# Performance work log

Hardware: AMD Instinct MI355X
Metric: run time of the kernel (lower is better)

Reference implementation:

```python
import jax, jax.numpy as jnp
import numpy as np

THRESHOLD = 0.95


def setup_inputs() -> dict:
    key = jax.random.key(0)
    k1, k2 = jax.random.split(key, 2)
    B, T, D = 16, 2048, 1024
    hs = jax.random.normal(k1, (B, T, D), dtype=jnp.float32)
    hs_mask = jnp.ones((B, 1, T), dtype=jnp.float32)
    w = jax.random.normal(k2, (D,), dtype=jnp.float32) * 0.02  # project.weight [1,D] -> [D]
    b = jnp.zeros((), dtype=jnp.float32)                        # project.bias
    return {"hs": hs, "hs_mask": hs_mask, "w": w, "b": b}


def reference(hs, hs_mask, w, b):
    B, T, D = hs.shape
    # project + sigmoid + mask
    x = jnp.einsum("btd,d->bt", hs, w) + b            # [B,T]
    alphas_s = jax.nn.sigmoid(x)
    alphas = alphas_s * hs_mask[:, 0, :]              # [B,T]

    # ---- integrate-and-fire scan over time ----
    def step(carry, inp):
        integrate, frame = carry                      # [B], [B,D]
        alpha, h = inp                                # [B], [B,D]
        dist_completion = 1.0 - integrate
        integrate = integrate + alpha
        fire_val = integrate                          # recorded pre-reset value
        fireplace = integrate > THRESHOLD
        integrate = jnp.where(fireplace, integrate - 1.0, integrate)
        cur = jnp.where(fireplace, dist_completion, alpha)
        frame_out = frame + cur[:, None] * h          # recorded frame at t
        frame_next = jnp.where(fireplace[:, None], (alpha - cur)[:, None] * h, frame_out)
        return (integrate, frame_next), (fire_val, frame_out)

    init = (jnp.zeros((B,), hs.dtype), jnp.zeros((B, D), hs.dtype))
    _, (fires_t, frames_t) = jax.lax.scan(
        step, init, (jnp.swapaxes(alphas, 0, 1), jnp.swapaxes(hs, 0, 1)))
    fires = jnp.swapaxes(fires_t, 0, 1)               # [B,T]
    frames = jnp.swapaxes(frames_t, 0, 1)             # [B,T,D]

    # ---- gather fired frames, left-packed, padded to static L=T ----
    fired = fires > THRESHOLD                         # [B,T]
    pos = jnp.cumsum(fired.astype(jnp.int32), axis=1) - 1
    L = T                                             # static upper bound on label length
    pos = jnp.where(fired, pos, L)                    # out-of-range -> dropped
    bidx = jnp.broadcast_to(jnp.arange(B, dtype=jnp.int32)[:, None], (B, T))
    out = jnp.zeros((B, L, D), hs.dtype).at[bidx, pos].set(frames, mode="drop")

    len_labels = jnp.round(alphas.sum(-1)).astype(jnp.int32)          # [B]
    new_masks = (jnp.arange(L)[None, :] < len_labels[:, None])[:, None, :]  # [B,1,L] bool
    return out, new_masks
```

## Files before the change

### kernel.cpp

```cpp
#include <hip/hip_runtime.h>
#include <math.h>

#define BB 16
#define TT 2048
#define DD 1024
#define THRESH 0.95f

__global__ __launch_bounds__(256) void proj_kernel(
    const float* __restrict__ hs, const float* __restrict__ hs_mask,
    const float* __restrict__ w, const float* __restrict__ bias,
    float* __restrict__ alphas)
{
    int row  = blockIdx.x * 4 + (threadIdx.x >> 6);
    int lane = threadIdx.x & 63;
    const float4* hp = (const float4*)(hs + (size_t)row * DD);
    const float4* wp = (const float4*)w;
    float sum = 0.f;
#pragma unroll
    for (int j = 0; j < 4; ++j) {
        float4 h4 = hp[lane + 64 * j];
        float4 w4 = wp[lane + 64 * j];
        sum += h4.x * w4.x + h4.y * w4.y + h4.z * w4.z + h4.w * w4.w;
    }
#pragma unroll
    for (int off = 32; off; off >>= 1) sum += __shfl_down(sum, off, 64);
    if (lane == 0) {
        float x  = sum + bias[0];
        float al = 1.f / (1.f + expf(-x));
        alphas[row] = al * hs_mask[row];
    }
}


#define SCAN_GROUP(RREG, GIDX)                                                \
    {                                                                         \
        float cv = 0.f, pv = 0.f;                                             \
        _Pragma("unroll 16")                                                  \
        for (int j = 0; j < 64; ++j) {                                        \
            float a = __int_as_float(                                         \
                __builtin_amdgcn_readlane(__float_as_int(RREG), j));          \
            float pre  = integ + a;                         \
            bool  fire = pre > THRESH;                      \
            float c    = fire ? dist : a;                                     \
            integ      = fire ? pre - 1.f : pre;        \
            dist       = 1.f - integ;                                         \
            bool sel   = (lane == j);                                         \
            cv = sel ? c   : cv;                                              \
            pv = sel ? pre : pv;                                              \
        }                                                                     \
        cp[(GIDX) * 64 + lane] = cv;                                          \
        unsigned long long bm = __ballot(pv > THRESH);                        \
        gmask = (lane == (GIDX)) ? bm : gmask;                                \
    }

__global__ __launch_bounds__(64) void scan_kernel(
    const float* __restrict__ alphas, float* __restrict__ cur,
    int* __restrict__ fire_times, int* __restrict__ n_fires,
    int* __restrict__ len_labels)
{
    int b    = blockIdx.x;
    int lane = threadIdx.x;
    const float* ap = alphas + (size_t)b * TT;
    float*       cp = cur    + (size_t)b * TT;

    unsigned long long gmask = 0ull;
    float integ = 0.f, dist = 1.f;
    double dsum = 0.0;

    for (int outer = 0; outer < 4; ++outer) {
        int base = outer * 512 + lane;
        float r0 = ap[base +   0];
        float r1 = ap[base +  64];
        float r2 = ap[base + 128];
        float r3 = ap[base + 192];
        float r4 = ap[base + 256];
        float r5 = ap[base + 320];
        float r6 = ap[base + 384];
        float r7 = ap[base + 448];
        dsum += (double)r0 + (double)r1 + (double)r2 + (double)r3
              + (double)r4 + (double)r5 + (double)r6 + (double)r7;
        int gb = outer * 8;
        SCAN_GROUP(r0, gb + 0)
        SCAN_GROUP(r1, gb + 1)
        SCAN_GROUP(r2, gb + 2)
        SCAN_GROUP(r3, gb + 3)
        SCAN_GROUP(r4, gb + 4)
        SCAN_GROUP(r5, gb + 5)
        SCAN_GROUP(r6, gb + 6)
        SCAN_GROUP(r7, gb + 7)
    }

#pragma unroll
    for (int off = 32; off; off >>= 1) dsum += __shfl_down(dsum, off, 64);
    if (lane == 0) len_labels[b] = (int)__double2int_rn(dsum);

    int cnt  = __popcll(gmask);
    int pref = cnt;
#pragma unroll
    for (int off = 1; off < 64; off <<= 1) {
        int y = __shfl_up(pref, off, 64);
        if (lane >= off) pref += y;
    }
    int pos = pref - cnt;
    unsigned long long m = gmask;
    int baset = lane * 64;
    int* fp = fire_times + (size_t)b * TT;
    while (m) {
        int j = __ffsll(m) - 1;
        fp[pos++] = baset + j;
        m &= m - 1;
    }
    if (lane == 63) n_fires[b] = pref;
}

__global__ __launch_bounds__(256) void gather_kernel(
    const float* __restrict__ hs, const float* __restrict__ alphas,
    const float* __restrict__ cur, const int* __restrict__ fire_times,
    const int* __restrict__ n_fires, const int* __restrict__ len_labels,
    float* __restrict__ out, float* __restrict__ out_mask)
{
    int ro = blockIdx.x;
    int b  = ro >> 11;
    int r  = ro & (TT - 1);
    if (threadIdx.x == 0)
        out_mask[ro] = (r < len_labels[b]) ? 1.f : 0.f;

    float4* op = (float4*)(out + (size_t)ro * DD);
    int ti = threadIdx.x;
    if (r >= n_fires[b]) {
        float4 z = {0.f, 0.f, 0.f, 0.f};
        op[ti] = z;
        return;
    }
    int t_end  = fire_times[b * TT + r];
    int t_prev = r ? fire_times[b * TT + r - 1] : -1;

    const float4* hsb = (const float4*)(hs + (size_t)b * TT * DD);
    float4 acc = {0.f, 0.f, 0.f, 0.f};
    if (t_prev >= 0) {
        float c = alphas[b * TT + t_prev] - cur[b * TT + t_prev];
        float4 h = hsb[(size_t)t_prev * 256 + ti];
        acc.x += c * h.x; acc.y += c * h.y; acc.z += c * h.z; acc.w += c * h.w;
    }
    for (int t = t_prev + 1; t <= t_end; ++t) {
        float c = cur[b * TT + t];
        float4 h = hsb[(size_t)t * 256 + ti];
        acc.x += c * h.x; acc.y += c * h.y; acc.z += c * h.z; acc.w += c * h.w;
    }
    op[ti] = acc;
}

extern "C" void kernel_launch(void* const* d_in, const int* in_sizes, int n_in,
                              void* d_out, int out_size, void* d_ws, size_t ws_size,
                              hipStream_t stream) {
    const float* hs      = (const float*)d_in[0];
    const float* hs_mask = (const float*)d_in[1];
    const float* w       = (const float*)d_in[2];
    const float* bias    = (const float*)d_in[3];

    float* out      = (float*)d_out;
    float* out_mask = out + (size_t)BB * TT * DD;

    float* alphas     = (float*)d_ws;
    float* cur        = alphas + BB * TT;
    int*   fire_times = (int*)(cur + BB * TT);
    int*   n_fires    = fire_times + BB * TT;
    int*   len_labels = n_fires + BB;

    proj_kernel<<<BB * TT / 4, 256, 0, stream>>>(hs, hs_mask, w, bias, alphas);
    scan_kernel<<<BB, 64, 0, stream>>>(alphas, cur, fire_times, n_fires, len_labels);
    gather_kernel<<<BB * TT, 256, 0, stream>>>(hs, alphas, cur, fire_times,
                                               n_fires, len_labels, out, out_mask);
}
```

Measured before the change: 309.0 us.

## Process multiple output rows per gather block, reuse boundary frame, nontemporal stores

The gather kernel now handles 8 consecutive output rows per block. It walks the time range once and carries the boundary hidden row and its leftover weight from one fired frame to the next, so that row is not reloaded from memory. Output writes use nontemporal stores to avoid polluting the cache with the large output, and mask generation moves into the scan kernel. The trade-off is fewer, longer-running blocks with a serial dependency chain inside each block, which may cut parallelism and memory-level overlap.

```diff
diff --git a/kernel.cpp b/kernel.cpp
--- a/kernel.cpp
+++ b/kernel.cpp
@@ -5,6 +5,14 @@
 #define TT 2048
 #define DD 1024
 #define THRESH 0.95f
+#define RPB 8
+
+typedef float nt4 __attribute__((ext_vector_type(4)));
+
+__device__ __forceinline__ void nt_store4(const float4& v, float4* p) {
+    nt4 x = {v.x, v.y, v.z, v.w};
+    __builtin_nontemporal_store(x, (nt4*)p);
+}
 
 __global__ __launch_bounds__(256) void proj_kernel(
     const float* __restrict__ hs, const float* __restrict__ hs_mask,
@@ -56,7 +64,7 @@
 __global__ __launch_bounds__(64) void scan_kernel(
     const float* __restrict__ alphas, float* __restrict__ cur,
     int* __restrict__ fire_times, int* __restrict__ n_fires,
-    int* __restrict__ len_labels)
+    int* __restrict__ len_labels, float* __restrict__ out_mask)
 {
     int b    = blockIdx.x;
     int lane = threadIdx.x;
@@ -92,7 +100,14 @@
 
 #pragma unroll
     for (int off = 32; off; off >>= 1) dsum += __shfl_down(dsum, off, 64);
-    if (lane == 0) len_labels[b] = (int)__double2int_rn(dsum);
+    int len = __double2int_rn(dsum);
+    len = __shfl(len, 0, 64);
+    if (lane == 0) len_labels[b] = len;
+
+    float* mp = out_mask + (size_t)b * TT;
+#pragma unroll
+    for (int j = 0; j < TT / 64; ++j)
+        mp[j * 64 + lane] = ((j * 64 + lane) < len) ? 1.f : 0.f;
 
     int cnt  = __popcll(gmask);
     int pref = cnt;
@@ -116,38 +131,71 @@
 __global__ __launch_bounds__(256) void gather_kernel(
     const float* __restrict__ hs, const float* __restrict__ alphas,
     const float* __restrict__ cur, const int* __restrict__ fire_times,
-    const int* __restrict__ n_fires, const int* __restrict__ len_labels,
-    float* __restrict__ out, float* __restrict__ out_mask)
+    const int* __restrict__ n_fires, float* __restrict__ out)
 {
-    int ro = blockIdx.x;
-    int b  = ro >> 11;
-    int r  = ro & (TT - 1);
-    if (threadIdx.x == 0)
-        out_mask[ro] = (r < len_labels[b]) ? 1.f : 0.f;
-
-    float4* op = (float4*)(out + (size_t)ro * DD);
+    int chunk = blockIdx.x;
+    int b  = chunk >> 8;
+    int r0 = (chunk & 255) * RPB;
     int ti = threadIdx.x;
-    if (r >= n_fires[b]) {
+    int nf = n_fires[b];
+
+    float4* ob = (float4*)(out + ((size_t)b * TT + r0) * DD);
+
+    if (r0 >= nf) {
         float4 z = {0.f, 0.f, 0.f, 0.f};
-        op[ti] = z;
+#pragma unroll
+        for (int i = 0; i < RPB; ++i)
+            nt_store4(z, &ob[i * 256 + ti]);
         return;
     }
-    int t_end  = fire_times[b * TT + r];
-    int t_prev = r ? fire_times[b * TT + r - 1] : -1;
-
+
+    const int*    ft  = fire_times + (size_t)b * TT;
+    const float*  al  = alphas     + (size_t)b * TT;
+    const float*  cu  = cur        + (size_t)b * TT;
     const float4* hsb = (const float4*)(hs + (size_t)b * TT * DD);
-    float4 acc = {0.f, 0.f, 0.f, 0.f};
-    if (t_prev >= 0) {
-        float c = alphas[b * TT + t_prev] - cur[b * TT + t_prev];
-        float4 h = hsb[(size_t)t_prev * 256 + ti];
-        acc.x += c * h.x; acc.y += c * h.y; acc.z += c * h.z; acc.w += c * h.w;
-    }
-    for (int t = t_prev + 1; t <= t_end; ++t) {
-        float c = cur[b * TT + t];
-        float4 h = hsb[(size_t)t * 256 + ti];
-        acc.x += c * h.x; acc.y += c * h.y; acc.z += c * h.z; acc.w += c * h.w;
-    }
-    op[ti] = acc;
+
+    int    t;
+    float4 hprev = {0.f, 0.f, 0.f, 0.f};
+    float  wprev = 0.f;
+    bool   have_prev;
+    if (r0 == 0) {
+        t = 0;
+        have_prev = false;
+    } else {
+        int tp = ft[r0 - 1];
+        t = tp + 1;
+        hprev = hsb[(size_t)tp * 256 + ti];
+        wprev = al[tp] - cu[tp];
+        have_prev = true;
+    }
+
+#pragma unroll
+    for (int i = 0; i < RPB; ++i) {
+        int r = r0 + i;
+        float4 a = {0.f, 0.f, 0.f, 0.f};
+        if (r < nf) {
+            if (have_prev) {
+                a.x = wprev * hprev.x; a.y = wprev * hprev.y;
+                a.z = wprev * hprev.z; a.w = wprev * hprev.w;
+            }
+            int te = ft[r];
+            for (;;) {
+                float4 h  = hsb[(size_t)t * 256 + ti];
+                float  cw = cu[t];
+                a.x += cw * h.x; a.y += cw * h.y;
+                a.z += cw * h.z; a.w += cw * h.w;
+                if (t == te) {
+                    wprev = al[t] - cw;
+                    hprev = h;
+                    ++t;
+                    break;
+                }
+                ++t;
+            }
+            have_prev = true;
+        }
+        nt_store4(a, &ob[i * 256 + ti]);
+    }
 }
 
 extern "C" void kernel_launch(void* const* d_in, const int* in_sizes, int n_in,
@@ -168,7 +216,8 @@
     int*   len_labels = n_fires + BB;
 
     proj_kernel<<<BB * TT / 4, 256, 0, stream>>>(hs, hs_mask, w, bias, alphas);
-    scan_kernel<<<BB, 64, 0, stream>>>(alphas, cur, fire_times, n_fires, len_labels);
-    gather_kernel<<<BB * TT, 256, 0, stream>>>(hs, alphas, cur, fire_times,
-                                               n_fires, len_labels, out, out_mask);
-}
+    scan_kernel<<<BB, 64, 0, stream>>>(alphas, cur, fire_times, n_fires,
+                                       len_labels, out_mask);
+    gather_kernel<<<BB * (TT / RPB), 256, 0, stream>>>(hs, alphas, cur, fire_times,
+                                                       n_fires, out);
+}
```

Result: faster. 302.8 us (-2.0%).
